# Performance work log

Measured on AMD Instinct MI355X. Metric: run time of the kernel, lower is better.

Reference implementation:

```python
import jax, jax.numpy as jnp
import numpy as np

DIM = 512
HEADS = 8
DIM_HEAD = 64
INNER = HEADS * DIM_HEAD  # 512
B, N = 4, 2048


def setup_inputs() -> dict:
    key = jax.random.key(0)
    k1, k2, k3, k4 = jax.random.split(key, 4)
    x = jax.random.normal(k1, (B, N, DIM), dtype=jnp.float32)
    # nn.Linear(dim, inner*3, bias=False): weight [3*inner, dim]; store transposed [dim, 3*inner]
    w_qkv = jax.random.normal(k2, (DIM, 3 * INNER), dtype=jnp.float32) / np.sqrt(DIM)
    w_out = jax.random.normal(k3, (INNER, DIM), dtype=jnp.float32) / np.sqrt(INNER)
    b_out = jax.random.normal(k4, (DIM,), dtype=jnp.float32) * 0.01
    return {"x": x, "w_qkv": w_qkv, "w_out": w_out, "b_out": b_out}


def reference(x, w_qkv, w_out, b_out):
    b, n, _ = x.shape
    scale = DIM_HEAD ** -0.5
    qkv = x @ w_qkv  # [b, n, 3*inner]
    q, k, v = jnp.split(qkv, 3, axis=-1)
    # [b, n, h, d] -> [b, h, n, d]
    reshape = lambda t: t.reshape(b, n, HEADS, DIM_HEAD).transpose(0, 2, 1, 3)
    q, k, v = reshape(q), reshape(k), reshape(v)
    dots = jnp.einsum('bhid,bhjd->bhij', q, k) * scale  # [b, h, n, n]
    attn = jax.nn.softmax(dots, axis=-1)
    out = jnp.einsum('bhij,bhjd->bhid', attn, v)  # [b, h, n, d]
    out = out.transpose(0, 2, 1, 3).reshape(b, n, INNER)
    return out @ w_out + b_out  # dropout is identity at inference
```

## Files before the change

### kernel.cpp

```cpp
#include <hip/hip_runtime.h>
#include <hip/hip_bf16.h>
#include <cstdint>

#define DEV __device__ __forceinline__

typedef __attribute__((ext_vector_type(8))) __bf16 bf16x8;
typedef __attribute__((ext_vector_type(4))) float floatx4;
typedef __attribute__((ext_vector_type(4))) short shortx4;
typedef __attribute__((ext_vector_type(8))) short shortx8;

constexpr float QSCALE = 0.18033688011112042f;

DEV unsigned short f2b(float f) {
  union { float f; unsigned u; } v; v.f = f;
  return (unsigned short)((v.u + 0x7fffu + ((v.u >> 16) & 1u)) >> 16);
}

#if defined(__has_builtin) && __has_builtin(__builtin_amdgcn_cvt_pk_bf16_f32)
DEV unsigned pk2(float a, float b) {
  typedef __attribute__((ext_vector_type(2))) __bf16 bf2;
  union { bf2 v; unsigned u; } u;
  u.v = __builtin_amdgcn_cvt_pk_bf16_f32(a, b);
  return u.u;
}
#else
DEV unsigned pk2(float a, float b) {
  return (unsigned)f2b(a) | ((unsigned)f2b(b) << 16);
}
#endif

#if defined(__has_builtin) && __has_builtin(__builtin_amdgcn_exp2f)
DEV float fexp2(float x) { return __builtin_amdgcn_exp2f(x); }
#else
DEV float fexp2(float x) { return exp2f(x); }
#endif

DEV floatx4 mfma16(bf16x8 a, bf16x8 b, floatx4 c) {
  return __builtin_amdgcn_mfma_f32_16x16x32_bf16(a, b, c, 0, 0, 0);
}

#define GLD_LDS16(gp, lp)                                                          \
  __builtin_amdgcn_global_load_lds(                                                \
      (const __attribute__((address_space(1))) void*)(gp),                         \
      (__attribute__((address_space(3))) void*)(lp), 16, 0, 0)

__global__ void tcvt2(const float* __restrict__ w_qkv,
                      const float* __restrict__ w_out,
                      unsigned short* __restrict__ wqkvt,
                      unsigned short* __restrict__ woutt) {
  __shared__ float tile[32][33];
  const float* in; unsigned short* out; int C, bx;
  if (blockIdx.x < 48) { in = w_qkv; out = wqkvt; C = 1536; bx = blockIdx.x; }
  else { in = w_out; out = woutt; C = 512; bx = blockIdx.x - 48; }
  const int R = 512;
  int tx = threadIdx.x & 31, ty = threadIdx.x >> 5;
  int r0 = blockIdx.y * 32, c0 = bx * 32;
#pragma unroll
  for (int i = 0; i < 4; i++) {
    int rr = ty + i * 8;
    tile[rr][tx] = in[(size_t)(r0 + rr) * C + c0 + tx];
  }
  __syncthreads();
#pragma unroll
  for (int i = 0; i < 4; i++) {
    int rr = ty + i * 8;
    out[(size_t)(c0 + rr) * R + r0 + tx] = f2b(tile[tx][rr]);
  }
}

__global__ __launch_bounds__(256, 3) void gemm_qkv(
    const float* __restrict__ x, const unsigned short* __restrict__ Bt,
    unsigned short* __restrict__ qf, unsigned short* __restrict__ kf,
    unsigned short* __restrict__ vf) {
  __shared__ __align__(16) char smem[49152];
  const int tid = threadIdx.x;
  const int lane = tid & 63, wid = tid >> 6;
  const int g = lane >> 4, r = lane & 15;
  const int m0 = blockIdx.y * 128, n0 = blockIdx.x * 128;
  const int wm = (wid & 1) * 64, wn = (wid >> 1) * 64;

  floatx4 acc[4][4] = {};

  int rA[4], kA[4];
#pragma unroll
  for (int i = 0; i < 4; i++) {
    int c = i * 256 + tid;
    rA[i] = c >> 3;
    kA[i] = (c & 7) ^ (rA[i] & 7);
  }
  int rB[2], kB[2];
#pragma unroll
  for (int i = 0; i < 2; i++) {
    int c = i * 256 + tid;
    rB[i] = c >> 2;
    kB[i] = (c & 3) ^ ((rB[i] >> 1) & 3);
  }

#define STAGE_G(kt, b)                                                           \
  {                                                                              \
    _Pragma("unroll") for (int i = 0; i < 4; i++)                                \
        GLD_LDS16(x + (size_t)(m0 + rA[i]) * 512 + (kt) + kA[i] * 4,             \
                  smem + (b)*16384 + i * 4096 + wid * 1024);                     \
    _Pragma("unroll") for (int i = 0; i < 2; i++)                                \
        GLD_LDS16(Bt + (size_t)(n0 + rB[i]) * 512 + (kt) + kB[i] * 8,            \
                  smem + 32768 + (b)*8192 + i * 4096 + wid * 1024);              \
  }

  STAGE_G(0, 0)
  for (int it = 0; it < 16; it++) {
    const int buf = it & 1;
    __syncthreads();
    if (it + 1 < 16) STAGE_G((it + 1) * 32, buf ^ 1)
    const float* Af = (const float*)(smem + buf * 16384);
    const unsigned short* Ws = (const unsigned short*)(smem + 32768 + buf * 8192);
    bf16x8 a[4], b[4];
#pragma unroll
    for (int t = 0; t < 4; t++) {
      int rw = wm + t * 16 + r;
      const float* Ar = Af + rw * 32;
      floatx4 f0 = *(const floatx4*)(Ar + (((2 * g)) ^ (rw & 7)) * 4);
      floatx4 f1 = *(const floatx4*)(Ar + (((2 * g + 1)) ^ (rw & 7)) * 4);
      union { unsigned u[4]; bf16x8 v; } w;
      w.u[0] = pk2(f0[0], f0[1]); w.u[1] = pk2(f0[2], f0[3]);
      w.u[2] = pk2(f1[0], f1[1]); w.u[3] = pk2(f1[2], f1[3]);
      a[t] = w.v;
      int rb = wn + t * 16 + r;
      b[t] = *(const bf16x8*)(Ws + rb * 32 + (g ^ ((rb >> 1) & 3)) * 8);
    }
#pragma unroll
    for (int mt = 0; mt < 4; mt++)
#pragma unroll
      for (int nt = 0; nt < 4; nt++)
        acc[mt][nt] = mfma16(a[mt], b[nt], acc[mt][nt]);
  }
#undef STAGE_G

  const int which = blockIdx.x >> 2;
  if (which == 2) {
    const int tokbase = m0 + wm;
    const int bb = tokbase >> 11, vt = (tokbase & 2047) >> 6;
#pragma unroll
    for (int nt = 0; nt < 4; nt++) {
      int vcol = n0 + wn + nt * 16 + r - 1024;
      int h = vcol >> 6;
      size_t hb = (size_t)(bb * 8 + h) * 131072 + (size_t)vt * 4096 + nt * 1024 +
                  (g * 16 + r) * 8;
#pragma unroll
      for (int kc = 0; kc < 2; kc++) {
        union { unsigned u[4]; shortx8 v; } w;
        w.u[0] = pk2(acc[2 * kc][nt][0], acc[2 * kc][nt][1]);
        w.u[1] = pk2(acc[2 * kc][nt][2], acc[2 * kc][nt][3]);
        w.u[2] = pk2(acc[2 * kc + 1][nt][0], acc[2 * kc + 1][nt][1]);
        w.u[3] = pk2(acc[2 * kc + 1][nt][2], acc[2 * kc + 1][nt][3]);
        *(shortx8*)(vf + hb + kc * 512) = w.v;
      }
    }
  } else {
    const float sc = (which == 0) ? QSCALE : 1.f;
    unsigned short* dst = (which == 0) ? qf : kf;
    unsigned short* sm = (unsigned short*)smem;
    __syncthreads();
#pragma unroll
    for (int mt = 0; mt < 4; mt++)
#pragma unroll
      for (int nt = 0; nt < 4; nt++) {
        int col = wn + nt * 16 + r;
#pragma unroll
        for (int e = 0; e < 4; e++)
          sm[(wm + mt * 16 + g * 4 + e) * 136 + col] = f2b(acc[mt][nt][e] * sc);
      }
    __syncthreads();
#pragma unroll
    for (int it = 0; it < 8; it++) {
      int c = it * 256 + tid;
      int row = c >> 4, cc = c & 15;
      shortx8 v = *(const shortx8*)(sm + row * 136 + cc * 8);
      int gq = n0 + cc * 8;
      int h = (gq >> 6) & 7, d0 = gq & 63;
      int kc = d0 >> 5, gp = (d0 >> 3) & 3;
      int tok = m0 + row, bb = tok >> 11, n = tok & 2047;
      *(shortx8*)(dst + (size_t)(bb * 8 + h) * 131072 + (n >> 4) * 1024 +
                  kc * 512 + (gp * 16 + (n & 15)) * 8) = v;
    }
  }
}

__global__ __launch_bounds__(256, 2) void gemm_out(
    const unsigned short* __restrict__ A, const unsigned short* __restrict__ Bt,
    float* __restrict__ outF, const float* __restrict__ bias) {
  __shared__ __align__(16) unsigned short smem[16896];
  const int tid = threadIdx.x;
  const int lane = tid & 63, wid = tid >> 6;
  const int g = lane >> 4, r = lane & 15;
  const int m0 = blockIdx.y * 64, n0 = blockIdx.x * 128;
  const int wn = wid * 32;
  const int K = 512;

  floatx4 acc[4][2] = {};

  const int rA = tid >> 2, kA = (tid & 3) ^ ((rA >> 1) & 3);
  int rB[2], kB[2];
#pragma unroll
  for (int i = 0; i < 2; i++) {
    int c = i * 256 + tid;
    rB[i] = c >> 2;
    kB[i] = (c & 3) ^ ((rB[i] >> 1) & 3);
  }

#define STAGE_O(kt, b)                                                           \
  {                                                                              \
    GLD_LDS16(A + (size_t)(m0 + rA) * K + (kt) + kA * 8,                         \
              (char*)smem + (b)*4096 + wid * 1024);                              \
    _Pragma("unroll") for (int i = 0; i < 2; i++)                                \
        GLD_LDS16(Bt + (size_t)(n0 + rB[i]) * K + (kt) + kB[i] * 8,              \
                  (char*)smem + 8192 + (b)*8192 + i * 4096 + wid * 1024);        \
  }

  STAGE_O(0, 0)
  for (int it = 0; it < 16; it++) {
    const int buf = it & 1;
    __syncthreads();
    if (it + 1 < 16) STAGE_O((it + 1) * 32, buf ^ 1)
    const unsigned short* Xs = smem + buf * 2048;
    const unsigned short* Ws = smem + 4096 + buf * 4096;
    bf16x8 a[4], b[2];
#pragma unroll
    for (int t = 0; t < 4; t++) {
      int rw = t * 16 + r;
      a[t] = *(const bf16x8*)(Xs + rw * 32 + (g ^ ((rw >> 1) & 3)) * 8);
    }
#pragma unroll
    for (int t = 0; t < 2; t++) {
      int rb = wn + t * 16 + r;
      b[t] = *(const bf16x8*)(Ws + rb * 32 + (g ^ ((rb >> 1) & 3)) * 8);
    }
#pragma unroll
    for (int mt = 0; mt < 4; mt++)
#pragma unroll
      for (int bt = 0; bt < 2; bt++)
        acc[mt][bt] = mfma16(a[mt], b[bt], acc[mt][bt]);
  }
#undef STAGE_O

  float* ftile = (float*)smem;
  __syncthreads();
#pragma unroll
  for (int mt = 0; mt < 4; mt++)
#pragma unroll
    for (int bt = 0; bt < 2; bt++)
#pragma unroll
      for (int e = 0; e < 4; e++)
        ftile[(mt * 16 + g * 4 + e) * 132 + wn + bt * 16 + r] = acc[mt][bt][e];
  __syncthreads();
#pragma unroll
  for (int it = 0; it < 8; it++) {
    int c = it * 256 + tid;
    int lr = c >> 5, cc = c & 31;
    floatx4 v = *(const floatx4*)(ftile + lr * 132 + cc * 4);
    int col = n0 + cc * 4;
    v += *(const floatx4*)(bias + col);
    *(floatx4*)(outF + (size_t)(m0 + lr) * 512 + col) = v;
  }
}

__global__ __launch_bounds__(256, 2) void attn(
    const unsigned short* __restrict__ qf, const unsigned short* __restrict__ kf,
    const unsigned short* __restrict__ vf, unsigned short* __restrict__ ao) {
  __shared__ __align__(16) unsigned short Osm[4][32 * 72];
  const int tid = threadIdx.x, lane = tid & 63, wid = tid >> 6;
  const int g = lane >> 4, r = lane & 15;
  const int bh = blockIdx.x;
  const size_t fbase = (size_t)bh * 131072;
  const unsigned short* kb = kf + fbase;
  const unsigned short* vb = vf + fbase;
  const int q0 = blockIdx.y * 128 + wid * 32;
  const int qt0 = q0 >> 4;

  bf16x8 bq[2][2];
#pragma unroll
  for (int nt = 0; nt < 2; nt++)
#pragma unroll
    for (int kc = 0; kc < 2; kc++)
      bq[nt][kc] = *(const bf16x8*)(qf + fbase + (size_t)(qt0 + nt) * 1024 +
                                    kc * 512 + lane * 8);

  floatx4 o[2][4] = {};
  float lsum[2] = {0.f, 0.f};

  bf16x8 akA[4][2], bvA[4][2], akB[4][2], bvB[4][2];

#define LOADKV(ak_, bv_, s_)                                                     \
  {                                                                              \
    const size_t kt = (size_t)(s_)*4096;                                         \
    _Pragma("unroll") for (int mt = 0; mt < 4; mt++)                             \
      _Pragma("unroll") for (int kc = 0; kc < 2; kc++)                           \
          ak_[mt][kc] = *(const bf16x8*)(kb + kt + mt * 1024 + kc * 512 +        \
                                         lane * 8);                              \
    _Pragma("unroll") for (int b = 0; b < 4; b++)                                \
      _Pragma("unroll") for (int kc = 0; kc < 2; kc++)                           \
          bv_[b][kc] = *(const bf16x8*)(vb + kt + b * 1024 + kc * 512 +          \
                                        lane * 8);                               \
  }

#define STEP(akC, bvC, akN, bvN, sn, cond)                                       \
  {                                                                              \
    if (cond) LOADKV(akN, bvN, sn)                                               \
    _Pragma("unroll") for (int nt = 0; nt < 2; nt++) {                           \
      floatx4 st[4] = {};                                                        \
      _Pragma("unroll") for (int kc = 0; kc < 2; kc++)                           \
        _Pragma("unroll") for (int mt = 0; mt < 4; mt++)                         \
            st[mt] = mfma16(akC[mt][kc], bq[nt][kc], st[mt]);                    \
      float p[4][4];                                                             \
      _Pragma("unroll") for (int mt = 0; mt < 4; mt++)                           \
        _Pragma("unroll") for (int e = 0; e < 4; e++)                            \
            p[mt][e] = fexp2(st[mt][e]);                                         \
      lsum[nt] += ((p[0][0] + p[0][1]) + (p[0][2] + p[0][3])) +                  \
                  ((p[1][0] + p[1][1]) + (p[1][2] + p[1][3])) +                  \
                  ((p[2][0] + p[2][1]) + (p[2][2] + p[2][3])) +                  \
                  ((p[3][0] + p[3][1]) + (p[3][2] + p[3][3]));                   \
      bf16x8 ap[2];                                                              \
      _Pragma("unroll") for (int kc = 0; kc < 2; kc++) {                         \
        union { unsigned u[4]; bf16x8 v; } w;                                    \
        w.u[0] = pk2(p[2 * kc][0], p[2 * kc][1]);                                \
        w.u[1] = pk2(p[2 * kc][2], p[2 * kc][3]);                                \
        w.u[2] = pk2(p[2 * kc + 1][0], p[2 * kc + 1][1]);                        \
        w.u[3] = pk2(p[2 * kc + 1][2], p[2 * kc + 1][3]);                        \
        ap[kc] = w.v;                                                            \
      }                                                                          \
      _Pragma("unroll") for (int kc = 0; kc < 2; kc++)                           \
        _Pragma("unroll") for (int b = 0; b < 4; b++)                            \
            o[nt][b] = mfma16(ap[kc], bvC[b][kc], o[nt][b]);                     \
    }                                                                            \
  }

  LOADKV(akA, bvA, 0)
  for (int s2 = 0; s2 < 16; s2++) {
    STEP(akA, bvA, akB, bvB, 2 * s2 + 1, true)
    STEP(akB, bvB, akA, bvA, 2 * s2 + 2, s2 < 15)
  }
#undef STEP
#undef LOADKV

#pragma unroll
  for (int nt = 0; nt < 2; nt++) {
    lsum[nt] += __shfl_xor(lsum[nt], 16);
    lsum[nt] += __shfl_xor(lsum[nt], 32);
  }

#pragma unroll
  for (int nt = 0; nt < 2; nt++) {
    float il[4];
#pragma unroll
    for (int e = 0; e < 4; e++) il[e] = 1.f / __shfl(lsum[nt], g * 4 + e);
#pragma unroll
    for (int b = 0; b < 4; b++)
#pragma unroll
      for (int e = 0; e < 4; e++)
        Osm[wid][(nt * 16 + g * 4 + e) * 72 + b * 16 + r] =
            f2b(o[nt][b][e] * il[e]);
  }
  __syncthreads();
  const int bb = bh >> 3, h = bh & 7;
#pragma unroll
  for (int it = 0; it < 4; it++) {
    int c = it * 256 + tid;
    int row = c >> 3, cc = c & 7;
    int w = row >> 5, r5 = row & 31;
    shortx8 v = *(const shortx8*)(&Osm[w][r5 * 72 + cc * 8]);
    int tok = blockIdx.y * 128 + row;
    *(shortx8*)(ao + ((size_t)(bb * 2048 + tok)) * 512 + h * 64 + cc * 8) = v;
  }
}

extern "C" void kernel_launch(void* const* d_in, const int* in_sizes, int n_in,
                              void* d_out, int out_size, void* d_ws, size_t ws_size,
                              hipStream_t stream) {
  const float* x = (const float*)d_in[0];
  const float* w_qkv = (const float*)d_in[1];
  const float* w_out = (const float*)d_in[2];
  const float* b_out = (const float*)d_in[3];
  float* out = (float*)d_out;

  unsigned short* wsp = (unsigned short*)d_ws;
  unsigned short* wqkvt = wsp;
  unsigned short* woutt = wqkvt + (size_t)1536 * 512;
  unsigned short* qf = woutt + (size_t)512 * 512;
  unsigned short* kf = qf + (size_t)32 * 2048 * 64;
  unsigned short* vf = kf + (size_t)32 * 2048 * 64;
  unsigned short* ao = vf + (size_t)32 * 2048 * 64;

  tcvt2<<<dim3(64, 16), 256, 0, stream>>>(w_qkv, w_out, wqkvt, woutt);
  gemm_qkv<<<dim3(12, 64), 256, 0, stream>>>(x, wqkvt, qf, kf, vf);
  attn<<<dim3(32, 16), 256, 0, stream>>>(qf, kf, vf, ao);
  gemm_out<<<dim3(4, 128), 256, 0, stream>>>(ao, woutt, out, b_out);
}
```

Baseline: 159.5 us.

## Compute softmax row sums via MFMA with ones and restructure K/V prefetch

Replaces the per-lane VALU summation of exponentials and the cross-lane shuffle reduction with an extra MFMA against a vector of ones, so row sums accumulate directly in the output layout. The attention loop is also reorganised: only K is double-buffered in registers, V is loaded just-in-time inside each step after the QK MFMAs, and block-wide barriers are added between steps to keep waves in lockstep for cache reuse. This frees VGPRs and VALU work, at the cost of extra MFMA instructions, less latency hiding for V loads, and barrier stalls.

```diff
diff --git a/kernel.cpp b/kernel.cpp
--- a/kernel.cpp
+++ b/kernel.cpp
@@ -284,74 +284,80 @@
       bq[nt][kc] = *(const bf16x8*)(qf + fbase + (size_t)(qt0 + nt) * 1024 +
                                     kc * 512 + lane * 8);
 
+  bf16x8 vones;
+#pragma unroll
+  for (int i = 0; i < 8; i++) vones[i] = (__bf16)1.0f;
+
   floatx4 o[2][4] = {};
-  float lsum[2] = {0.f, 0.f};
-
-  bf16x8 akA[4][2], bvA[4][2], akB[4][2], bvB[4][2];
-
-#define LOADKV(ak_, bv_, s_)                                                     \
+  floatx4 lacc[2] = {};
+
+  bf16x8 akA[4][2], akB[4][2];
+
+#define LOADK(ak_, s_)                                                           \
   {                                                                              \
     const size_t kt = (size_t)(s_)*4096;                                         \
     _Pragma("unroll") for (int mt = 0; mt < 4; mt++)                             \
       _Pragma("unroll") for (int kc = 0; kc < 2; kc++)                           \
           ak_[mt][kc] = *(const bf16x8*)(kb + kt + mt * 1024 + kc * 512 +        \
                                          lane * 8);                              \
-    _Pragma("unroll") for (int b = 0; b < 4; b++)                                \
-      _Pragma("unroll") for (int kc = 0; kc < 2; kc++)                           \
-          bv_[b][kc] = *(const bf16x8*)(vb + kt + b * 1024 + kc * 512 +          \
-                                        lane * 8);                               \
-  }
-
-#define STEP(akC, bvC, akN, bvN, sn, cond)                                       \
+  }
+
+#define STEPC(akC, s_)                                                           \
   {                                                                              \
-    if (cond) LOADKV(akN, bvN, sn)                                               \
+    floatx4 st[2][4] = {};                                                       \
+    _Pragma("unroll") for (int kc = 0; kc < 2; kc++)                             \
+      _Pragma("unroll") for (int mt = 0; mt < 4; mt++)                           \
+        _Pragma("unroll") for (int nt = 0; nt < 2; nt++)                         \
+            st[nt][mt] = mfma16(akC[mt][kc], bq[nt][kc], st[nt][mt]);            \
+                    \
+    bf16x8 bv[4][2];                                                             \
+    {                                                                            \
+      const size_t vt = (size_t)(s_)*4096;                                       \
+      _Pragma("unroll") for (int b = 0; b < 4; b++)                              \
+        _Pragma("unroll") for (int kc = 0; kc < 2; kc++)                         \
+            bv[b][kc] = *(const bf16x8*)(vb + vt + b * 1024 + kc * 512 +         \
+                                         lane * 8);                              \
+    }                                                                            \
+    bf16x8 ap[2][2];                                                             \
     _Pragma("unroll") for (int nt = 0; nt < 2; nt++) {                           \
-      floatx4 st[4] = {};                                                        \
-      _Pragma("unroll") for (int kc = 0; kc < 2; kc++)                           \
-        _Pragma("unroll") for (int mt = 0; mt < 4; mt++)                         \
-            st[mt] = mfma16(akC[mt][kc], bq[nt][kc], st[mt]);                    \
       float p[4][4];                                                             \
       _Pragma("unroll") for (int mt = 0; mt < 4; mt++)                           \
         _Pragma("unroll") for (int e = 0; e < 4; e++)                            \
-            p[mt][e] = fexp2(st[mt][e]);                                         \
-      lsum[nt] += ((p[0][0] + p[0][1]) + (p[0][2] + p[0][3])) +                  \
-                  ((p[1][0] + p[1][1]) + (p[1][2] + p[1][3])) +                  \
-                  ((p[2][0] + p[2][1]) + (p[2][2] + p[2][3])) +                  \
-                  ((p[3][0] + p[3][1]) + (p[3][2] + p[3][3]));                   \
-      bf16x8 ap[2];                                                              \
+            p[mt][e] = fexp2(st[nt][mt][e]);                                     \
       _Pragma("unroll") for (int kc = 0; kc < 2; kc++) {                         \
         union { unsigned u[4]; bf16x8 v; } w;                                    \
         w.u[0] = pk2(p[2 * kc][0], p[2 * kc][1]);                                \
         w.u[1] = pk2(p[2 * kc][2], p[2 * kc][3]);                                \
         w.u[2] = pk2(p[2 * kc + 1][0], p[2 * kc + 1][1]);                        \
         w.u[3] = pk2(p[2 * kc + 1][2], p[2 * kc + 1][3]);                        \
-        ap[kc] = w.v;                                                            \
+        ap[nt][kc] = w.v;                                                        \
       }                                                                          \
-      _Pragma("unroll") for (int kc = 0; kc < 2; kc++)                           \
+    }                                                                            \
+    _Pragma("unroll") for (int kc = 0; kc < 2; kc++)                             \
+      _Pragma("unroll") for (int nt = 0; nt < 2; nt++) {                         \
+        lacc[nt] = mfma16(ap[nt][kc], vones, lacc[nt]);                          \
         _Pragma("unroll") for (int b = 0; b < 4; b++)                            \
-            o[nt][b] = mfma16(ap[kc], bvC[b][kc], o[nt][b]);                     \
-    }                                                                            \
-  }
-
-  LOADKV(akA, bvA, 0)
+            o[nt][b] = mfma16(ap[nt][kc], bv[b][kc], o[nt][b]);                  \
+      }                                                                          \
+  }
+
+  LOADK(akA, 0)
   for (int s2 = 0; s2 < 16; s2++) {
-    STEP(akA, bvA, akB, bvB, 2 * s2 + 1, true)
-    STEP(akB, bvB, akA, bvA, 2 * s2 + 2, s2 < 15)
-  }
-#undef STEP
-#undef LOADKV
+    LOADK(akB, 2 * s2 + 1)
+    __builtin_amdgcn_s_barrier();
+    STEPC(akA, 2 * s2)
+    if (s2 < 15) LOADK(akA, 2 * s2 + 2)
+    __builtin_amdgcn_s_barrier();
+    STEPC(akB, 2 * s2 + 1)
+  }
+#undef STEPC
+#undef LOADK
 
 #pragma unroll
   for (int nt = 0; nt < 2; nt++) {
-    lsum[nt] += __shfl_xor(lsum[nt], 16);
-    lsum[nt] += __shfl_xor(lsum[nt], 32);
-  }
-
-#pragma unroll
-  for (int nt = 0; nt < 2; nt++) {
-    float il[4];
-#pragma unroll
-    for (int e = 0; e < 4; e++) il[e] = 1.f / __shfl(lsum[nt], g * 4 + e);
+    floatx4 il;
+#pragma unroll
+    for (int e = 0; e < 4; e++) il[e] = 1.f / lacc[nt][e];
 #pragma unroll
     for (int b = 0; b < 4; b++)
 #pragma unroll
```

Measured after the change: 167.3 us. 4.9% more time.
